# Optimization experiments

Measured on AMD Instinct MI355X. Metric: run time of the kernel, lower is better.

## Reference

```python
import jax, jax.numpy as jnp
import numpy as np

B, NPG = 64, 512          # graphs, nodes per graph
N_TOTAL = B * NPG
LIG = 128                 # ligand nodes per graph (segment 0); rest are protein (segment 1)
BOX = 40.0                # Angstrom box for random coords -> realistic radius-graph density
INTER_CUTOFF = 10.0       # normalize_coord is identity (scale=1)
INTRA_CUTOFF = 8.0


def setup_inputs() -> dict:
    key = jax.random.key(0)
    X = jax.random.uniform(key, (N_TOTAL, 1, 3), dtype=jnp.float32) * BOX
    batch_id = jnp.repeat(jnp.arange(B, dtype=jnp.int32), NPG)
    local = jnp.tile(jnp.arange(NPG, dtype=jnp.int32), B)
    segment_id = (local >= LIG).astype(jnp.int32)
    is_global = jnp.logical_or(local == 0, local == LIG)  # one global node per segment
    return {"X": X, "batch_id": batch_id, "segment_id": segment_id, "is_global": is_global}


def _radial_edges(X, src_dst, cutoff):
    # src_dst: [E, 2] node indices; X: [N, C, 3], channel 0 holds coords
    p = X[:, 0][src_dst]                              # [E, 2, 3]
    dist = jnp.linalg.norm(p[:, 0] - p[:, 1], axis=-1)
    return src_dst[dist <= cutoff].T                  # [2, E']


def reference(X, batch_id, segment_id, is_global):
    N = batch_id.shape[0]
    nB = int(batch_id[-1]) + 1
    lengths = jax.ops.segment_sum(jnp.ones_like(batch_id), batch_id, num_segments=nB)
    max_n = int(jnp.max(lengths))
    offsets = jnp.concatenate([jnp.zeros((1,), lengths.dtype), jnp.cumsum(lengths)[:-1]])
    gni = jnp.arange(N)
    gni2lni = gni - offsets[batch_id]                 # local node index within its graph

    # Dense [N, max_n] same-batch mask via cumsum trick (O(N*max_n))
    same_bid = jnp.zeros((N, max_n), jnp.float32)
    same_bid = same_bid.at[gni, lengths[batch_id] - 1].set(1.0)
    same_bid = 1.0 - jnp.cumsum(same_bid, axis=-1)
    same_bid = jnp.concatenate([jnp.ones((N, 1), jnp.float32), same_bid[:, :-1]], axis=-1)
    same_bid = same_bid.at[gni, gni2lni].set(0.0)     # remove self edges

    row, col = jnp.nonzero(same_bid)                  # all same-graph candidate pairs
    col = col + offsets[batch_id[row]]                # local col -> global node index

    row_global = is_global[row]
    col_global = is_global[col]
    not_global = jnp.logical_not(jnp.logical_or(row_global, col_global))
    row_seg = segment_id[row]
    col_seg = segment_id[col]

    # intra-protein context edges (segment 1, within 8A)
    sel = (row_seg == col_seg) & (row_seg == 1) & not_global
    ctx_edges = _radial_edges(X, jnp.stack([row[sel], col[sel]], axis=1), INTRA_CUTOFF)

    # inter ligand-protein edges (within 10A)
    sel = (row_seg != col_seg) & not_global
    ir, ic = row[sel], col[sel]
    inter_edges = _radial_edges(X, jnp.stack([ir, ic], axis=1), INTER_CUTOFF)
    if inter_edges.shape[1] == 0:
        inter_edges = jnp.array([[ir[0], ic[0]], [ic[0], ir[0]]], dtype=inter_edges.dtype)

    reduced_inter_edge_batchid = batch_id[inter_edges[0][inter_edges[0] < inter_edges[1]]]
    reduced_inter_edge_offsets = offsets[reduced_inter_edge_batchid]

    # global<->same-segment edges and global<->global edges appended to context
    sel = (row_seg == col_seg) & jnp.logical_not(not_global)
    global_normal = jnp.stack([row[sel], col[sel]])
    sel = row_global & col_global
    global_global = jnp.stack([row[sel], col[sel]])
    ctx_edges = jnp.concatenate([ctx_edges, global_normal, global_global], axis=1)

    return ctx_edges, inter_edges, reduced_inter_edge_batchid, reduced_inter_edge_offsets
```

## Files before the change

### kernel.cpp

```cpp
#include <hip/hip_runtime.h>

#define NB 64
#define NPG 512
#define LIG 128
#define NBLK 512
#define RPB 64
#define THREADS 512

__device__ __forceinline__ bool dist_ok(float dx, float dy, float dz, float cutoff) {
    float s = __fadd_rn(__fadd_rn(__fmul_rn(dx, dx), __fmul_rn(dy, dy)), __fmul_rn(dz, dz));
    return __fsqrt_rn(s) <= cutoff;
}

__global__ __launch_bounds__(THREADS) void count_kernel(const float* __restrict__ X,
                                                        unsigned long long* __restrict__ gmask,
                                                        int* __restrict__ bp) {
    __shared__ float s[NPG * 3];
    __shared__ unsigned long long smask[RPB * 8];
    __shared__ int swc[8], swi[8];
    const int b = blockIdx.x;
    const int g = b >> 3;
    const int o = b & 7;
    const int t = threadIdx.x;
    const int lane = t & 63;
    const int w = t >> 6;
    if (t < 384) ((float4*)s)[t] = ((const float4*)X)[g * 384 + t];
    __syncthreads();

    int wc = 0, wi = 0;
    if (o < 2) {
        for (int j = 0; j < 8; ++j) {
            const int lr = w * 8 + j;
            const int r = o * 64 + lr;
            const float px = s[3 * r], py = s[3 * r + 1], pz = s[3 * r + 2];
            if (r != 0) {
                int ci = 0;
                for (int k = 2; k < 8; ++k) {
                    const int c = k * 64 + lane;
                    const bool pred = (c > LIG) &&
                        dist_ok(px - s[3 * c], py - s[3 * c + 1], pz - s[3 * c + 2], 10.0f);
                    const unsigned long long m = __ballot(pred);
                    if (lane == 0) smask[lr * 8 + k] = m;
                    ci += __popcll(m);
                }
                if (lane == 0) { smask[lr * 8 + 0] = 0; smask[lr * 8 + 1] = 0; }
                wi += ci;
            } else if (lane < 8) {
                smask[lr * 8 + lane] = 0;
            }
        }
    } else {
        for (int j = 0; j < 8; ++j) {
            const int lr = w * 8 + j;
            const int r = o * 64 + lr;
            const float px = s[3 * r], py = s[3 * r + 1], pz = s[3 * r + 2];
            if (r != LIG) {
                int ci = 0, cc = 0;
                for (int k = 0; k < 2; ++k) {
                    const int c = k * 64 + lane;
                    const bool pred = (c >= 1) && (c < LIG) &&
                        dist_ok(px - s[3 * c], py - s[3 * c + 1], pz - s[3 * c + 2], 10.0f);
                    const unsigned long long m = __ballot(pred);
                    if (lane == 0) smask[lr * 8 + k] = m;
                    ci += __popcll(m);
                }
                for (int k = 2; k < 8; ++k) {
                    const int c = k * 64 + lane;
                    const bool pred = (c > LIG) && (c != r) &&
                        dist_ok(px - s[3 * c], py - s[3 * c + 1], pz - s[3 * c + 2], 8.0f);
                    const unsigned long long m = __ballot(pred);
                    if (lane == 0) smask[lr * 8 + k] = m;
                    cc += __popcll(m);
                }
                wi += ci; wc += cc;
            } else if (lane < 8) {
                smask[lr * 8 + lane] = 0;
            }
        }
    }
    if (lane == 0) { swc[w] = wc; swi[w] = wi; }
    __syncthreads();
    gmask[(size_t)b * 512 + t] = smask[t];
    if (t == 0) {
        int c = 0, i = 0;
        for (int k = 0; k < 8; ++k) { c += swc[k]; i += swi[k]; }
        bp[b] = c;
        bp[NBLK + b] = i;
        bp[2 * NBLK + b] = (o < 2) ? i : 0;
    }
}

__global__ __launch_bounds__(THREADS) void emit_kernel(const unsigned long long* __restrict__ gmask,
                                                       const int* __restrict__ bp,
                                                       int* __restrict__ out) {
    __shared__ unsigned long long smask[RPB * 8];
    __shared__ int s0[NBLK], s1[NBLK], s2[NBLK];
    __shared__ int sc[RPB], si[RPB], sr[RPB];
    __shared__ int blkb[3], tot[3];
    const int b = blockIdx.x;
    const int g = b >> 3;
    const int o = b & 7;
    const int t = threadIdx.x;
    const int lane = t & 63;
    const int w = t >> 6;
    const unsigned long long lmask = (1ull << lane) - 1ull;
    const int gn = g * NPG;

    smask[t] = gmask[(size_t)b * 512 + t];
    const int vc = bp[t], vi = bp[NBLK + t], vr = bp[2 * NBLK + t];
    s0[t] = vc; s1[t] = vi; s2[t] = vr;
    __syncthreads();
    for (int off = 1; off < NBLK; off <<= 1) {
        int a0 = 0, a1 = 0, a2 = 0;
        if (t >= off) { a0 = s0[t - off]; a1 = s1[t - off]; a2 = s2[t - off]; }
        __syncthreads();
        s0[t] += a0; s1[t] += a1; s2[t] += a2;
        __syncthreads();
    }
    if (t == b) { blkb[0] = s0[t] - vc; blkb[1] = s1[t] - vi; blkb[2] = s2[t] - vr; }
    if (t == NBLK - 1) { tot[0] = s0[t]; tot[1] = s1[t]; tot[2] = s2[t]; }
    __syncthreads();

    int mc = 0, mi = 0, mr = 0;
    if (t < RPB) {
        if (o < 2) {
            for (int k = 2; k < 8; ++k) mi += __popcll(smask[t * 8 + k]);
            mr = mi;
        } else {
            mi = __popcll(smask[t * 8 + 0]) + __popcll(smask[t * 8 + 1]);
            for (int k = 2; k < 8; ++k) mc += __popcll(smask[t * 8 + k]);
        }
        sc[t] = mc; si[t] = mi; sr[t] = mr;
    }
    __syncthreads();
    for (int off = 1; off < RPB; off <<= 1) {
        int a0 = 0, a1 = 0, a2 = 0;
        if (t >= off && t < RPB) { a0 = sc[t - off]; a1 = si[t - off]; a2 = sr[t - off]; }
        __syncthreads();
        if (t < RPB) { sc[t] += a0; si[t] += a1; sr[t] += a2; }
        __syncthreads();
    }
    if (t < RPB) {
        sc[t] += blkb[0] - mc;
        si[t] += blkb[1] - mi;
        sr[t] += blkb[2] - mr;
    }
    __syncthreads();

    const int Eci = tot[0];
    const int Ei  = tot[1];
    const int Er  = tot[2];
    const int Ectx = Eci + NB * 1020 + NB * 2;

    int* ctx_src   = out;
    int* ctx_dst   = out + Ectx;
    int* inter_src = out + 2 * Ectx;
    int* inter_dst = inter_src + Ei;
    int* red_bid   = out + 2 * Ectx + 2 * Ei;
    int* red_off   = red_bid + Er;

    for (int j = 0; j < 8; ++j) {
        const int lr = w * 8 + j;
        const int r = o * 64 + lr;
        const int row = gn + r;

        if (o < 2) {
            if (r == 0) {
                for (int k = 0; k < 2; ++k) {
                    const int c = k * 64 + lane;
                    if (c >= 1 && c < LIG) {
                        const int pos = Eci + g * 1020 + (c - 1);
                        ctx_src[pos] = row; ctx_dst[pos] = gn + c;
                    }
                }
                if (lane == 0) {
                    const int pos = Eci + NB * 1020 + g * 2;
                    ctx_src[pos] = row; ctx_dst[pos] = gn + LIG;
                }
            } else {
                int ib = si[lr];
                int rb = sr[lr];
                for (int k = 2; k < 8; ++k) {
                    const unsigned long long m = smask[lr * 8 + k];
                    if ((m >> lane) & 1ull) {
                        const int c = k * 64 + lane;
                        const int p = __popcll(m & lmask);
                        inter_src[ib + p] = row; inter_dst[ib + p] = gn + c;
                        red_bid[rb + p] = g;     red_off[rb + p] = gn;
                    }
                    const int cnt = __popcll(m);
                    ib += cnt; rb += cnt;
                }
                if (lane == 0) {
                    const int pos = Eci + g * 1020 + (LIG - 1) + (r - 1);
                    ctx_src[pos] = row; ctx_dst[pos] = gn;
                }
            }
        } else {
            if (r == LIG) {
                for (int k = 2; k < 8; ++k) {
                    const int c = k * 64 + lane;
                    if (c > LIG) {
                        const int pos = Eci + g * 1020 + 2 * (LIG - 1) + (c - LIG - 1);
                        ctx_src[pos] = row; ctx_dst[pos] = gn + c;
                    }
                }
                if (lane == 0) {
                    const int pos = Eci + NB * 1020 + g * 2 + 1;
                    ctx_src[pos] = row; ctx_dst[pos] = gn;
                }
            } else {
                int ib = si[lr];
                for (int k = 0; k < 2; ++k) {
                    const unsigned long long m = smask[lr * 8 + k];
                    if ((m >> lane) & 1ull) {
                        const int c = k * 64 + lane;
                        const int pos = ib + __popcll(m & lmask);
                        inter_src[pos] = row; inter_dst[pos] = gn + c;
                    }
                    ib += __popcll(m);
                }
                int cb = sc[lr];
                for (int k = 2; k < 8; ++k) {
                    const unsigned long long m = smask[lr * 8 + k];
                    if ((m >> lane) & 1ull) {
                        const int c = k * 64 + lane;
                        const int pos = cb + __popcll(m & lmask);
                        ctx_src[pos] = row; ctx_dst[pos] = gn + c;
                    }
                    cb += __popcll(m);
                }
                if (lane == 0) {
                    const int pos = Eci + g * 1020 + 2 * (LIG - 1) + (NPG - LIG - 1) + (r - LIG - 1);
                    ctx_src[pos] = row; ctx_dst[pos] = gn + LIG;
                }
            }
        }
    }
}

extern "C" void kernel_launch(void* const* d_in, const int* in_sizes, int n_in,
                              void* d_out, int out_size, void* d_ws, size_t ws_size,
                              hipStream_t stream) {
    (void)in_sizes; (void)n_in; (void)out_size; (void)ws_size;
    const float* X = (const float*)d_in[0];
    int* ws = (int*)d_ws;
    int* bp = ws;
    unsigned long long* gmask =
        (unsigned long long*)(ws + 4096);
    int* out = (int*)d_out;

    count_kernel<<<NBLK, THREADS, 0, stream>>>(X, gmask, bp);
    emit_kernel<<<NBLK, THREADS, 0, stream>>>(gmask, bp, out);
}
```

Before: 89.39 us.

## Fuse count and emit kernels with a grid-wide atomic barrier

Merges the count and emit passes into one persistent-style kernel. Each block publishes its per-block counts to global memory, then spins on an atomic counter until all 512 blocks have arrived. This removes the second launch and the global round trip of the bit masks, and column coordinates are now cached in registers. It relies on all 512 blocks being co-resident, which can deadlock on smaller devices. It also adds a memset launch to reset the counter.

```diff
diff --git a/kernel.cpp b/kernel.cpp
--- a/kernel.cpp
+++ b/kernel.cpp
@@ -12,91 +12,17 @@
     return __fsqrt_rn(s) <= cutoff;
 }
 
-__global__ __launch_bounds__(THREADS) void count_kernel(const float* __restrict__ X,
-                                                        unsigned long long* __restrict__ gmask,
-                                                        int* __restrict__ bp) {
+__global__ __launch_bounds__(THREADS) void fused_kernel(const float* __restrict__ X,
+                                                        int* __restrict__ bp,
+                                                        unsigned int* __restrict__ cnt,
+                                                        int* __restrict__ out) {
     __shared__ float s[NPG * 3];
     __shared__ unsigned long long smask[RPB * 8];
-    __shared__ int swc[8], swi[8];
-    const int b = blockIdx.x;
-    const int g = b >> 3;
-    const int o = b & 7;
-    const int t = threadIdx.x;
-    const int lane = t & 63;
-    const int w = t >> 6;
-    if (t < 384) ((float4*)s)[t] = ((const float4*)X)[g * 384 + t];
-    __syncthreads();
-
-    int wc = 0, wi = 0;
-    if (o < 2) {
-        for (int j = 0; j < 8; ++j) {
-            const int lr = w * 8 + j;
-            const int r = o * 64 + lr;
-            const float px = s[3 * r], py = s[3 * r + 1], pz = s[3 * r + 2];
-            if (r != 0) {
-                int ci = 0;
-                for (int k = 2; k < 8; ++k) {
-                    const int c = k * 64 + lane;
-                    const bool pred = (c > LIG) &&
-                        dist_ok(px - s[3 * c], py - s[3 * c + 1], pz - s[3 * c + 2], 10.0f);
-                    const unsigned long long m = __ballot(pred);
-                    if (lane == 0) smask[lr * 8 + k] = m;
-                    ci += __popcll(m);
-                }
-                if (lane == 0) { smask[lr * 8 + 0] = 0; smask[lr * 8 + 1] = 0; }
-                wi += ci;
-            } else if (lane < 8) {
-                smask[lr * 8 + lane] = 0;
-            }
-        }
-    } else {
-        for (int j = 0; j < 8; ++j) {
-            const int lr = w * 8 + j;
-            const int r = o * 64 + lr;
-            const float px = s[3 * r], py = s[3 * r + 1], pz = s[3 * r + 2];
-            if (r != LIG) {
-                int ci = 0, cc = 0;
-                for (int k = 0; k < 2; ++k) {
-                    const int c = k * 64 + lane;
-                    const bool pred = (c >= 1) && (c < LIG) &&
-                        dist_ok(px - s[3 * c], py - s[3 * c + 1], pz - s[3 * c + 2], 10.0f);
-                    const unsigned long long m = __ballot(pred);
-                    if (lane == 0) smask[lr * 8 + k] = m;
-                    ci += __popcll(m);
-                }
-                for (int k = 2; k < 8; ++k) {
-                    const int c = k * 64 + lane;
-                    const bool pred = (c > LIG) && (c != r) &&
-                        dist_ok(px - s[3 * c], py - s[3 * c + 1], pz - s[3 * c + 2], 8.0f);
-                    const unsigned long long m = __ballot(pred);
-                    if (lane == 0) smask[lr * 8 + k] = m;
-                    cc += __popcll(m);
-                }
-                wi += ci; wc += cc;
-            } else if (lane < 8) {
-                smask[lr * 8 + lane] = 0;
-            }
-        }
-    }
-    if (lane == 0) { swc[w] = wc; swi[w] = wi; }
-    __syncthreads();
-    gmask[(size_t)b * 512 + t] = smask[t];
-    if (t == 0) {
-        int c = 0, i = 0;
-        for (int k = 0; k < 8; ++k) { c += swc[k]; i += swi[k]; }
-        bp[b] = c;
-        bp[NBLK + b] = i;
-        bp[2 * NBLK + b] = (o < 2) ? i : 0;
-    }
-}
-
-__global__ __launch_bounds__(THREADS) void emit_kernel(const unsigned long long* __restrict__ gmask,
-                                                       const int* __restrict__ bp,
-                                                       int* __restrict__ out) {
-    __shared__ unsigned long long smask[RPB * 8];
+    __shared__ int rc[RPB], ri[RPB];
+    __shared__ int sc[RPB], si[RPB], sr[RPB];
     __shared__ int s0[NBLK], s1[NBLK], s2[NBLK];
-    __shared__ int sc[RPB], si[RPB], sr[RPB];
     __shared__ int blkb[3], tot[3];
+
     const int b = blockIdx.x;
     const int g = b >> 3;
     const int o = b & 7;
@@ -106,9 +32,88 @@
     const unsigned long long lmask = (1ull << lane) - 1ull;
     const int gn = g * NPG;
 
-    smask[t] = gmask[(size_t)b * 512 + t];
-    const int vc = bp[t], vi = bp[NBLK + t], vr = bp[2 * NBLK + t];
-    s0[t] = vc; s1[t] = vi; s2[t] = vr;
+    if (t < 384) ((float4*)s)[t] = ((const float4*)X)[g * 384 + t];
+    __syncthreads();
+
+    float cx[8], cy[8], cz[8];
+#pragma unroll
+    for (int k = 0; k < 8; ++k) {
+        const int c = k * 64 + lane;
+        cx[k] = s[3 * c]; cy[k] = s[3 * c + 1]; cz[k] = s[3 * c + 2];
+    }
+
+    for (int j = 0; j < 8; ++j) {
+        const int lr = w * 8 + j;
+        const int r = o * 64 + lr;
+        const float px = s[3 * r], py = s[3 * r + 1], pz = s[3 * r + 2];
+        int cc = 0, ci = 0;
+        if (o < 2) {
+            if (r != 0) {
+#pragma unroll
+                for (int k = 2; k < 8; ++k) {
+                    const int c = k * 64 + lane;
+                    const bool pred = (c > LIG) &&
+                        dist_ok(px - cx[k], py - cy[k], pz - cz[k], 10.0f);
+                    const unsigned long long m = __ballot(pred);
+                    if (lane == 0) smask[lr * 8 + k] = m;
+                    ci += __popcll(m);
+                }
+            }
+        } else {
+            if (r != LIG) {
+#pragma unroll
+                for (int k = 0; k < 2; ++k) {
+                    const int c = k * 64 + lane;
+                    const bool pred = (c >= 1) && (c < LIG) &&
+                        dist_ok(px - cx[k], py - cy[k], pz - cz[k], 10.0f);
+                    const unsigned long long m = __ballot(pred);
+                    if (lane == 0) smask[lr * 8 + k] = m;
+                    ci += __popcll(m);
+                }
+#pragma unroll
+                for (int k = 2; k < 8; ++k) {
+                    const int c = k * 64 + lane;
+                    const bool pred = (c > LIG) && (c != r) &&
+                        dist_ok(px - cx[k], py - cy[k], pz - cz[k], 8.0f);
+                    const unsigned long long m = __ballot(pred);
+                    if (lane == 0) smask[lr * 8 + k] = m;
+                    cc += __popcll(m);
+                }
+            }
+        }
+        if (lane == 0) { rc[lr] = cc; ri[lr] = ci; }
+    }
+    __syncthreads();
+
+    int mc = 0, mi = 0, mr = 0;
+    if (t < RPB) {
+        mc = rc[t]; mi = ri[t]; mr = (o < 2) ? mi : 0;
+        sc[t] = mc; si[t] = mi; sr[t] = mr;
+    }
+    __syncthreads();
+    for (int off = 1; off < RPB; off <<= 1) {
+        int a0 = 0, a1 = 0, a2 = 0;
+        if (t >= off && t < RPB) { a0 = sc[t - off]; a1 = si[t - off]; a2 = sr[t - off]; }
+        __syncthreads();
+        if (t < RPB) { sc[t] += a0; si[t] += a1; sr[t] += a2; }
+        __syncthreads();
+    }
+
+    if (t == 0) {
+        __hip_atomic_store(&bp[b],            sc[RPB - 1], __ATOMIC_RELAXED, __HIP_MEMORY_SCOPE_AGENT);
+        __hip_atomic_store(&bp[NBLK + b],     si[RPB - 1], __ATOMIC_RELAXED, __HIP_MEMORY_SCOPE_AGENT);
+        __hip_atomic_store(&bp[2 * NBLK + b], sr[RPB - 1], __ATOMIC_RELAXED, __HIP_MEMORY_SCOPE_AGENT);
+        __hip_atomic_fetch_add(cnt, 1u, __ATOMIC_RELEASE, __HIP_MEMORY_SCOPE_AGENT);
+        while (__hip_atomic_load(cnt, __ATOMIC_ACQUIRE, __HIP_MEMORY_SCOPE_AGENT) < NBLK) {
+            __builtin_amdgcn_s_sleep(2);
+        }
+    }
+    __syncthreads();
+
+    const int v0 = __hip_atomic_load(&bp[t],            __ATOMIC_RELAXED, __HIP_MEMORY_SCOPE_AGENT);
+    const int v1 = __hip_atomic_load(&bp[NBLK + t],     __ATOMIC_RELAXED, __HIP_MEMORY_SCOPE_AGENT);
+    const int v2 = __hip_atomic_load(&bp[2 * NBLK + t], __ATOMIC_RELAXED, __HIP_MEMORY_SCOPE_AGENT);
+    s0[t] = v0; s1[t] = v1; s2[t] = v2;
     __syncthreads();
     for (int off = 1; off < NBLK; off <<= 1) {
         int a0 = 0, a1 = 0, a2 = 0;
@@ -117,29 +122,10 @@
         s0[t] += a0; s1[t] += a1; s2[t] += a2;
         __syncthreads();
     }
-    if (t == b) { blkb[0] = s0[t] - vc; blkb[1] = s1[t] - vi; blkb[2] = s2[t] - vr; }
+    if (t == b) { blkb[0] = s0[t] - v0; blkb[1] = s1[t] - v1; blkb[2] = s2[t] - v2; }
     if (t == NBLK - 1) { tot[0] = s0[t]; tot[1] = s1[t]; tot[2] = s2[t]; }
     __syncthreads();
 
-    int mc = 0, mi = 0, mr = 0;
-    if (t < RPB) {
-        if (o < 2) {
-            for (int k = 2; k < 8; ++k) mi += __popcll(smask[t * 8 + k]);
-            mr = mi;
-        } else {
-            mi = __popcll(smask[t * 8 + 0]) + __popcll(smask[t * 8 + 1]);
-            for (int k = 2; k < 8; ++k) mc += __popcll(smask[t * 8 + k]);
-        }
-        sc[t] = mc; si[t] = mi; sr[t] = mr;
-    }
-    __syncthreads();
-    for (int off = 1; off < RPB; off <<= 1) {
-        int a0 = 0, a1 = 0, a2 = 0;
-        if (t >= off && t < RPB) { a0 = sc[t - off]; a1 = si[t - off]; a2 = sr[t - off]; }
-        __syncthreads();
-        if (t < RPB) { sc[t] += a0; si[t] += a1; sr[t] += a2; }
-        __syncthreads();
-    }
     if (t < RPB) {
         sc[t] += blkb[0] - mc;
         si[t] += blkb[1] - mi;
@@ -188,8 +174,8 @@
                         inter_src[ib + p] = row; inter_dst[ib + p] = gn + c;
                         red_bid[rb + p] = g;     red_off[rb + p] = gn;
                     }
-                    const int cnt = __popcll(m);
-                    ib += cnt; rb += cnt;
+                    const int cntm = __popcll(m);
+                    ib += cntm; rb += cntm;
                 }
                 if (lane == 0) {
                     const int pos = Eci + g * 1020 + (LIG - 1) + (r - 1);
@@ -246,10 +232,9 @@
     const float* X = (const float*)d_in[0];
     int* ws = (int*)d_ws;
     int* bp = ws;
-    unsigned long long* gmask =
-        (unsigned long long*)(ws + 4096);
+    unsigned int* cnt = (unsigned int*)(ws + 3 * NBLK);
     int* out = (int*)d_out;
 
-    count_kernel<<<NBLK, THREADS, 0, stream>>>(X, gmask, bp);
-    emit_kernel<<<NBLK, THREADS, 0, stream>>>(gmask, bp, out);
+    hipMemsetAsync(cnt, 0, sizeof(unsigned int), stream);
+    fused_kernel<<<NBLK, THREADS, 0, stream>>>(X, bp, cnt, out);
 }
```

Result: slower. 114.4 us (+28.0%).
